# Optimization experiments

Measured on AMD Instinct MI355X. Metric: run time of the kernel, lower is better.

## Reference

```python
import jax, jax.numpy as jnp
import numpy as np

B, S, E, H = 4, 1024, 1024, 16
D = E // H  # head_dim = 64


def setup_inputs() -> dict:
    key = jax.random.key(0)
    ks = jax.random.split(key, 12)
    s = 1.0 / np.sqrt(E)
    return {
        "query": jax.random.normal(ks[0], (B, S, E), jnp.float32),
        "key_": jax.random.normal(ks[1], (B, S, E), jnp.float32),
        "value": jax.random.normal(ks[2], (B, S, E), jnp.float32),
        "mask": jnp.ones((B, S, S), dtype=bool),
        "Wq": jax.random.uniform(ks[3], (E, E), jnp.float32, -s, s),
        "bq": jax.random.uniform(ks[4], (E,), jnp.float32, -s, s),
        "Wk": jax.random.uniform(ks[5], (E, E), jnp.float32, -s, s),
        "bk": jax.random.uniform(ks[6], (E,), jnp.float32, -s, s),
        "Wv": jax.random.uniform(ks[7], (E, E), jnp.float32, -s, s),
        "bv": jax.random.uniform(ks[8], (E,), jnp.float32, -s, s),
        "Wo": jax.random.uniform(ks[9], (E, E), jnp.float32, -s, s),
        "bo": jax.random.uniform(ks[10], (E,), jnp.float32, -s, s),
    }


def reference(query, key_, value, mask, Wq, bq, Wk, bk, Wv, bv, Wo, bo):
    # project and split heads: [B,S,E] -> [B,H,S,D]
    def heads(x, W, b):
        return (x @ W + b).reshape(B, -1, H, D).transpose(0, 2, 1, 3)

    q = heads(query, Wq, bq)
    k = heads(key_, Wk, bk)
    v = heads(value, Wv, bv)

    scores = jnp.einsum("bhqd,bhkd->bhqk", q, k) / jnp.sqrt(jnp.float32(D))
    # bool mask: positions where mask==0 are filled with -1e9
    scores = jnp.where(mask[:, None, :, :], scores, jnp.float32(-1e9))
    attn_weights = jax.nn.softmax(scores, axis=-1)  # [B,H,Sq,Sk]
    out = jnp.einsum("bhqk,bhkd->bhqd", attn_weights, v)
    out = out.transpose(0, 2, 1, 3).reshape(B, -1, E)  # [B,Sq,E]
    attn_output = out @ Wo + bo
    return attn_output, attn_weights
```

## Files before the change

### kernel.cpp

```cpp
#include <hip/hip_runtime.h>
#include <stdint.h>

typedef __bf16 bf16;
typedef bf16 bf16x2 __attribute__((ext_vector_type(2)));
typedef bf16 bf16x4 __attribute__((ext_vector_type(4)));
typedef bf16 bf16x8 __attribute__((ext_vector_type(8)));
typedef float f32x4 __attribute__((ext_vector_type(4)));
typedef float f32x16 __attribute__((ext_vector_type(16)));

static constexpr int Bc = 4, Sc = 1024, Ec = 1024, Hc = 16, Dc = 64, BSc = 4096;

__device__ __forceinline__ void gld_lds16(const void* g, void* s) {
  __builtin_amdgcn_global_load_lds((const __attribute__((address_space(1))) void*)g,
                                   (__attribute__((address_space(3))) void*)s, 16, 0, 0);
}

__global__ void detect_mask_kernel(const uint8_t* __restrict__ mask, int* flag) {
  if (threadIdx.x == 0 && blockIdx.x == 0) {
    bool everyGroupHasZero = true;
    bool anyNonzero = false;
    for (int j = 0; j < 16; ++j) {
      bool z = false;
      for (int bjj = 0; bjj < 4; ++bjj) {
        uint8_t byte = mask[4 * j + bjj];
        if (byte == 0) z = true;
        if (byte != 0) anyNonzero = true;
      }
      if (!z) everyGroupHasZero = false;
    }
    flag[0] = (everyGroupHasZero && anyNonzero) ? 4 : 1;
    flag[1] = 1;
  }
}

__global__ __launch_bounds__(256) void scan_mask_kernel(const uint8_t* __restrict__ mask,
                                                        int* __restrict__ mflag) {
  const int stride = mflag[0];
  bool ok = true;
  const uint4* p = (const uint4*)mask;
  if (stride == 1) {
    const int n = (Bc * Sc * Sc) / 16;
    for (int i = blockIdx.x * blockDim.x + threadIdx.x; i < n; i += gridDim.x * blockDim.x) {
      uint4 w = p[i];
      uint32_t z = 0;
      z |= (w.x - 0x01010101u) & ~w.x;
      z |= (w.y - 0x01010101u) & ~w.y;
      z |= (w.z - 0x01010101u) & ~w.z;
      z |= (w.w - 0x01010101u) & ~w.w;
      if (z & 0x80808080u) ok = false;
    }
  } else {
    const int n = (Bc * Sc * Sc) / 4;
    for (int i = blockIdx.x * blockDim.x + threadIdx.x; i < n; i += gridDim.x * blockDim.x) {
      uint4 w = p[i];
      if (w.x == 0u || w.y == 0u || w.z == 0u || w.w == 0u) ok = false;
    }
  }
  if (!ok) atomicAnd(&mflag[1], 0);
}

__global__ __launch_bounds__(256) void convert_x_kernel(
    const float* __restrict__ q, const float* __restrict__ k, const float* __restrict__ v,
    bf16* __restrict__ xb) {
  const int n4 = (BSc * Ec) / 4;
  for (int i = blockIdx.x * blockDim.x + threadIdx.x; i < 3 * n4; i += gridDim.x * blockDim.x) {
    int which = i / n4;
    int off = i - which * n4;
    const float4* src = (which == 0) ? (const float4*)q : (which == 1) ? (const float4*)k : (const float4*)v;
    float4 f = src[off];
    bf16x4 o;
    o[0] = (bf16)f.x; o[1] = (bf16)f.y; o[2] = (bf16)f.z; o[3] = (bf16)f.w;
    *(bf16x4*)(xb + (size_t)which * BSc * Ec + (size_t)off * 4) = o;
  }
}

__global__ __launch_bounds__(256) void convtrans_w_kernel(
    const float* __restrict__ Wq, const float* __restrict__ Wk,
    const float* __restrict__ Wv, const float* __restrict__ Wo,
    bf16* __restrict__ wT) {
  __shared__ float tile[64][65];
  const int k0 = blockIdx.x * 64, n0 = blockIdx.y * 64, z = blockIdx.z;
  const float* W = (z == 0) ? Wq : (z == 1) ? Wk : (z == 2) ? Wv : Wo;
  bf16* out = wT + (size_t)z * Ec * Ec;
  const int t = threadIdx.x;
#pragma unroll
  for (int p = 0; p < 16; p++) {
    int r = p * 4 + (t >> 6), c = t & 63;
    tile[r][c] = W[(size_t)(k0 + r) * Ec + n0 + c];
  }
  __syncthreads();
#pragma unroll
  for (int p = 0; p < 8; p++) {
    int n = p * 8 + (t >> 5), kk = (t & 31) * 2;
    bf16x2 v2;
    v2[0] = (bf16)tile[kk][n];
    v2[1] = (bf16)tile[kk + 1][n];
    *(bf16x2*)(out + (size_t)(n0 + n) * Ec + k0 + kk) = v2;
  }
}

template <int MODE>
__global__ __launch_bounds__(256) void gemm128_kernel(
    const bf16* __restrict__ A_, const bf16* __restrict__ W_,
    const float* __restrict__ bias0, const float* __restrict__ bias1, const float* __restrict__ bias2,
    bf16* __restrict__ outb_, float* __restrict__ outf) {
  constexpr int K = 1024, N = 1024;
  const int z = blockIdx.z;
  const bf16* A = A_ + (size_t)z * BSc * K;
  const bf16* Wt = W_ + (size_t)z * N * K;
  const float* bias = (z == 0) ? bias0 : (z == 1) ? bias1 : bias2;
  bf16* outb = outb_ + (size_t)z * Bc * Hc * Sc * Dc;
  const float oscale = (MODE == 1 && z == 0) ? 0.125f : 1.0f;
  const int n0 = blockIdx.x * 128, m0 = blockIdx.y * 128;

  __shared__ bf16 As[128 * 64];
  __shared__ bf16 Bs[128 * 64];
  const int t = threadIdx.x, wave = t >> 6, lane = t & 63;
  const int wr = wave >> 1, wc = wave & 1;

  f32x4 acc[4][4];
#pragma unroll
  for (int i = 0; i < 4; i++)
#pragma unroll
    for (int j = 0; j < 4; j++)
#pragma unroll
      for (int r = 0; r < 4; r++) acc[i][j][r] = 0.f;

  const int srow = (lane >> 3);
  const int scol = (lane & 7) * 8;

  for (int kt = 0; kt < K; kt += 64) {
#pragma unroll
    for (int i = 0; i < 4; i++) {
      const int chunk = i * 4 + wave;
      const int row = chunk * 8 + srow;
      gld_lds16(A + (size_t)(m0 + row) * K + kt + scol, &As[chunk * 512]);
      gld_lds16(Wt + (size_t)(n0 + row) * K + kt + scol, &Bs[chunk * 512]);
    }
    __syncthreads();
#pragma unroll
    for (int kk = 0; kk < 2; kk++) {
      bf16x8 af[4], bg[4];
#pragma unroll
      for (int i = 0; i < 4; i++) {
        af[i] = *(const bf16x8*)&As[(64 * wr + i * 16 + (lane & 15)) * 64 + kk * 32 + (lane >> 4) * 8];
        bg[i] = *(const bf16x8*)&Bs[(64 * wc + i * 16 + (lane & 15)) * 64 + kk * 32 + (lane >> 4) * 8];
      }
#pragma unroll
      for (int mi = 0; mi < 4; mi++)
#pragma unroll
        for (int ni = 0; ni < 4; ni++)
          acc[mi][ni] = __builtin_amdgcn_mfma_f32_16x16x32_bf16(af[mi], bg[ni], acc[mi][ni], 0, 0, 0);
    }
    __syncthreads();
  }

#pragma unroll
  for (int mi = 0; mi < 4; mi++) {
#pragma unroll
    for (int ni = 0; ni < 4; ni++) {
      const int col = n0 + 64 * wc + ni * 16 + (lane & 15);
      const float bvl = bias[col];
#pragma unroll
      for (int r = 0; r < 4; r++) {
        const int row = m0 + 64 * wr + mi * 16 + (lane >> 4) * 4 + r;
        const float v = (acc[mi][ni][r] + bvl) * oscale;
        if (MODE == 0) {
          outf[(size_t)row * N + col] = v;
        } else {
          const int bidx = row >> 10, s = row & 1023, hh = col >> 6, d = col & 63;
          const int dst = (z == 1) ? (d ^ ((s & 7) << 3)) : d;
          outb[(((size_t)bidx * Hc + hh) * Sc + s) * Dc + dst] = (bf16)v;
        }
      }
    }
  }
}

__global__ __launch_bounds__(256) void transpose_v_kernel(const bf16* __restrict__ Vb,
                                                          bf16* __restrict__ VTb) {
  __shared__ bf16 tile[64][66];
  const int s0 = blockIdx.x * 64, bh = blockIdx.y;
  const bf16* src = Vb + (size_t)bh * Sc * Dc;
  bf16* dst = VTb + (size_t)bh * Dc * Sc;
  const int t = threadIdx.x;
#pragma unroll
  for (int p = 0; p < 8; p++) {
    int s = p * 8 + (t >> 5), d = (t & 31) * 2;
    *(bf16x2*)&tile[s][d] = *(const bf16x2*)(src + (size_t)(s0 + s) * Dc + d);
  }
  __syncthreads();
#pragma unroll
  for (int p = 0; p < 8; p++) {
    int d = p * 8 + (t >> 5), s = (t & 31) * 2;
    bf16x2 v2;
    v2[0] = tile[s][d];
    v2[1] = tile[s + 1][d];
    const int sidx = (s0 + s) ^ ((d & 7) << 3);
    *(bf16x2*)(dst + (size_t)d * Sc + sidx) = v2;
  }
}

__device__ __forceinline__ f32x16 qk_lds(const char* sK, const bf16x8 qf[4],
                                         int koff, int l31, int hi) {
  const int row = koff + l31;
  const char* base = sK + row * 128;
  const int sw = (row & 7) << 4;
  f32x16 a;
#pragma unroll
  for (int r = 0; r < 16; r++) a[r] = 0.f;
#pragma unroll
  for (int ks = 0; ks < 4; ks++) {
    const bf16x8 kf = *(const bf16x8*)(base + ((ks * 32 + hi * 16) ^ sw));
    a = __builtin_amdgcn_mfma_f32_32x32x16_bf16(kf, qf[ks], a, 0, 0, 0);
  }
  return a;
}

__device__ __forceinline__ void mask_app(f32x16& a, int kt, const uint8_t* mrow1,
                                         const uint8_t* mrow4, int mstride, int hi) {
  if (mstride == 1) {
#pragma unroll
    for (int gg = 0; gg < 4; gg++) {
      const int kg = kt + gg * 8 + hi * 4;
      const uint32_t mw = *(const uint32_t*)(mrow1 + kg);
#pragma unroll
      for (int r = 0; r < 4; r++)
        if (((mw >> (8 * r)) & 0xffu) == 0u) a[gg * 4 + r] = -1e9f;
    }
  } else {
#pragma unroll
    for (int gg = 0; gg < 4; gg++) {
      const int kg = kt + gg * 8 + hi * 4;
      const uint4 m4 = *(const uint4*)(mrow4 + (size_t)4 * kg);
      const uint32_t w[4] = {m4.x, m4.y, m4.z, m4.w};
#pragma unroll
      for (int r = 0; r < 4; r++)
        if (w[r] == 0u) a[gg * 4 + r] = -1e9f;
    }
  }
}

__global__ __launch_bounds__(256, 3) void attn_kernel(
    const bf16* __restrict__ Qb, const bf16* __restrict__ Kb, const bf16* __restrict__ VTb,
    const uint8_t* __restrict__ mask, const int* __restrict__ mflag,
    float* __restrict__ wout_, bf16* __restrict__ ctx) {
  const int qg = blockIdx.x, h = blockIdx.y, b = blockIdx.z;
  const int bh = b * Hc + h;
  const int t = threadIdx.x, wave = t >> 6, lane = t & 63;
  const int l31 = lane & 31, hi = lane >> 5;
  const int q0 = qg * 128 + wave * 32;
  const int q = q0 + l31;

  __shared__ __attribute__((aligned(16))) char smem[49664];
  float* Pt = (float*)(smem + 32768) + wave * 1056;

  const bf16* Qp = Qb + ((size_t)bh * Sc + q) * Dc;
  bf16x8 qf[4];
#pragma unroll
  for (int ks = 0; ks < 4; ks++) qf[ks] = *(const bf16x8*)(Qp + ks * 16 + hi * 8);

  const int allTrue = mflag[1];
  const int mstride = mflag[0];
  const uint8_t* mrow1 = mask + (size_t)(b * Sc + q) * Sc;
  const uint8_t* mrow4 = mask + (size_t)(b * Sc + q) * Sc * 4;

  const char* Kbb = (const char*)(Kb + (size_t)bh * Sc * Dc);
  const char* VTbb = (const char*)(VTb + (size_t)bh * Dc * Sc);

  float m = -3.0e38f, l = 0.f;
  for (int st8 = 0; st8 < 8; st8++) {
#pragma unroll
    for (int j = 0; j < 4; j++) {
      const int off = j * 4096 + wave * 1024;
      gld_lds16(Kbb + st8 * 16384 + off + lane * 16, smem + off);
    }
    __syncthreads();
#pragma unroll
    for (int tl = 0; tl < 4; tl++) {
      f32x16 a = qk_lds(smem, qf, tl * 32, l31, hi);
      if (!allTrue) mask_app(a, st8 * 128 + tl * 32, mrow1, mrow4, mstride, hi);
      float tm = a[0];
#pragma unroll
      for (int r = 1; r < 16; r++) tm = fmaxf(tm, a[r]);
      const float mnew = fmaxf(m, tm);
      float s = 0.f;
#pragma unroll
      for (int r = 0; r < 16; r++) s += __expf(a[r] - mnew);
      l = l * __expf(m - mnew) + s;
      m = mnew;
    }
    __syncthreads();
  }
  {
    const float mo = __shfl_xor(m, 32), lo = __shfl_xor(l, 32);
    const float M = fmaxf(m, mo);
    l = l * __expf(m - M) + lo * __expf(mo - M);
    m = M;
  }
  const float invl = 1.f / l;

  float* wbase = wout_ + ((size_t)bh * Sc + q0) * Sc;
  f32x16 oacc[2];
#pragma unroll
  for (int nj = 0; nj < 2; nj++)
#pragma unroll
    for (int r = 0; r < 16; r++) oacc[nj][r] = 0.f;

  for (int st8 = 0; st8 < 8; st8++) {
#pragma unroll
    for (int j = 0; j < 4; j++) {
      const int off = j * 4096 + wave * 1024;
      gld_lds16(Kbb + st8 * 16384 + off + lane * 16, smem + off);
      const int goff = off + lane * 16;
      const int d = goff >> 8, ko = goff & 255;
      gld_lds16(VTbb + (size_t)d * 2048 + st8 * 256 + ko, smem + 16384 + off);
    }
    __syncthreads();
#pragma unroll
    for (int tl = 0; tl < 4; tl++) {
      f32x16 a = qk_lds(smem, qf, tl * 32, l31, hi);
      if (!allTrue) mask_app(a, st8 * 128 + tl * 32, mrow1, mrow4, mstride, hi);
#pragma unroll
      for (int gg = 0; gg < 4; gg++) {
        f32x4 w4;
#pragma unroll
        for (int r = 0; r < 4; r++) w4[r] = __expf(a[gg * 4 + r] - m) * invl;
        *(f32x4*)&Pt[l31 * 33 + gg * 8 + hi * 4] = w4;
      }
#pragma unroll
      for (int i = 0; i < 4; i++) {
        const int q2 = 8 * i + (lane >> 3), kk = (lane & 7) * 4;
        const f32x4 v4 = *(const f32x4*)&Pt[q2 * 33 + kk];
        __builtin_nontemporal_store(v4,
            (f32x4*)(wbase + (size_t)q2 * Sc + st8 * 128 + tl * 32 + kk));
      }
#pragma unroll
      for (int st = 0; st < 2; st++) {
        const f32x4 a0 = *(const f32x4*)&Pt[l31 * 33 + st * 16 + hi * 8];
        const f32x4 a1 = *(const f32x4*)&Pt[l31 * 33 + st * 16 + hi * 8 + 4];
        bf16x8 pa;
#pragma unroll
        for (int j = 0; j < 4; j++) {
          pa[j] = (bf16)a0[j];
          pa[4 + j] = (bf16)a1[j];
        }
#pragma unroll
        for (int nj = 0; nj < 2; nj++) {
          const int d = nj * 32 + l31;
          const int off = ((tl * 32 + st * 16 + hi * 8) * 2) ^ ((d & 7) << 4);
          const bf16x8 bv = *(const bf16x8*)(smem + 16384 + d * 256 + off);
          oacc[nj] = __builtin_amdgcn_mfma_f32_32x32x16_bf16(pa, bv, oacc[nj], 0, 0, 0);
        }
      }
    }
    __syncthreads();
  }

#pragma unroll
  for (int nj = 0; nj < 2; nj++) {
#pragma unroll
    for (int rg = 0; rg < 16; rg++) {
      const int qq = (rg & 3) + 8 * (rg >> 2) + 4 * hi;
      Pt[qq * 33 + l31] = oacc[nj][rg];
    }
    const int rr = lane >> 1, c0 = (lane & 1) * 16;
    bf16x8 o0, o1;
#pragma unroll
    for (int j = 0; j < 8; j++) {
      o0[j] = (bf16)Pt[rr * 33 + c0 + j];
      o1[j] = (bf16)Pt[rr * 33 + c0 + 8 + j];
    }
    bf16* cbase = ctx + ((size_t)(b * Sc + q0 + rr)) * Ec + h * Dc + nj * 32 + c0;
    *(bf16x8*)cbase = o0;
    *(bf16x8*)(cbase + 8) = o1;
  }
}

extern "C" void kernel_launch(void* const* d_in, const int* in_sizes, int n_in,
                              void* d_out, int out_size, void* d_ws, size_t ws_size,
                              hipStream_t stream) {
  const float* q = (const float*)d_in[0];
  const float* k = (const float*)d_in[1];
  const float* v = (const float*)d_in[2];
  const uint8_t* mask = (const uint8_t*)d_in[3];
  const float* Wq = (const float*)d_in[4];
  const float* bq = (const float*)d_in[5];
  const float* Wk = (const float*)d_in[6];
  const float* bk = (const float*)d_in[7];
  const float* Wv = (const float*)d_in[8];
  const float* bv = (const float*)d_in[9];
  const float* Wo = (const float*)d_in[10];
  const float* bo = (const float*)d_in[11];

  bf16* wsb = (bf16*)d_ws;
  bf16* xb = wsb;
  bf16* ctx = wsb;
  bf16* VTb = wsb + (size_t)4 * 1024 * 1024;
  bf16* wT = wsb + (size_t)12 * 1024 * 1024;
  bf16* Qb = wsb + (size_t)16 * 1024 * 1024;
  bf16* Kb = wsb + (size_t)20 * 1024 * 1024;
  bf16* Vb = wsb + (size_t)24 * 1024 * 1024;
  int* mflag = (int*)((char*)d_ws + (size_t)56 * 1024 * 1024);

  float* outf = (float*)d_out;
  float* attnw = outf + (size_t)4 * 1024 * 1024;

  detect_mask_kernel<<<1, 64, 0, stream>>>(mask, mflag);
  scan_mask_kernel<<<1024, 256, 0, stream>>>(mask, mflag);
  convert_x_kernel<<<2048, 256, 0, stream>>>(q, k, v, xb);
  convtrans_w_kernel<<<dim3(16, 16, 4), 256, 0, stream>>>(Wq, Wk, Wv, Wo, wT);
  gemm128_kernel<1><<<dim3(8, 32, 3), 256, 0, stream>>>(xb, wT, bq, bk, bv, Qb, nullptr);
  transpose_v_kernel<<<dim3(16, 64), 256, 0, stream>>>(Vb, VTb);
  attn_kernel<<<dim3(8, 16, 4), 256, 0, stream>>>(Qb, Kb, VTb, mask, mflag, attnw, ctx);
  gemm128_kernel<0><<<dim3(8, 32, 1), 256, 0, stream>>>(ctx, wT + (size_t)3 * 1024 * 1024,
                                                        bo, bo, bo, nullptr, outf);
}
```

Measured before the change: 224.4 us.

## Double-buffer K/V tiles in LDS and stage probabilities as bf16

The attention kernel now prefetches the next K tile (and V^T tile in the second pass) into an alternate LDS buffer while the current tile is processed. The goal is to overlap global loads with MFMA and softmax work instead of stalling at each barrier. The probability scratch and the output transpose buffer change from fp32 to bf16, which halves their LDS traffic and removes per-element conversions. In exchange, LDS per block grows to about 74 KB and occupancy drops from 3 to 2 blocks per CU. The fp32 attention weights written to global memory are now rounded through bf16, which lowers output precision.

```diff
diff --git a/kernel.cpp b/kernel.cpp
--- a/kernel.cpp
+++ b/kernel.cpp
@@ -241,7 +241,7 @@
   }
 }
 
-__global__ __launch_bounds__(256, 3) void attn_kernel(
+__global__ __launch_bounds__(256, 2) void attn_kernel(
     const bf16* __restrict__ Qb, const bf16* __restrict__ Kb, const bf16* __restrict__ VTb,
     const uint8_t* __restrict__ mask, const int* __restrict__ mflag,
     float* __restrict__ wout_, bf16* __restrict__ ctx) {
@@ -252,8 +252,8 @@
   const int q0 = qg * 128 + wave * 32;
   const int q = q0 + l31;
 
-  __shared__ __attribute__((aligned(16))) char smem[49664];
-  float* Pt = (float*)(smem + 32768) + wave * 1056;
+  __shared__ __attribute__((aligned(16))) char smem[75776];
+  bf16* Ptb = (bf16*)(smem + 65536) + wave * 1280;
 
   const bf16* Qp = Qb + ((size_t)bh * Sc + q) * Dc;
   bf16x8 qf[4];
@@ -269,16 +269,26 @@
   const char* VTbb = (const char*)(VTb + (size_t)bh * Dc * Sc);
 
   float m = -3.0e38f, l = 0.f;
+#pragma unroll
+  for (int j = 0; j < 4; j++) {
+    const int off = j * 4096 + wave * 1024;
+    gld_lds16(Kbb + off + lane * 16, smem + off);
+  }
+  __syncthreads();
   for (int st8 = 0; st8 < 8; st8++) {
-#pragma unroll
-    for (int j = 0; j < 4; j++) {
-      const int off = j * 4096 + wave * 1024;
-      gld_lds16(Kbb + st8 * 16384 + off + lane * 16, smem + off);
-    }
-    __syncthreads();
+    const int cur = st8 & 1;
+    if (st8 < 7) {
+#pragma unroll
+      for (int j = 0; j < 4; j++) {
+        const int off = j * 4096 + wave * 1024;
+        gld_lds16(Kbb + (st8 + 1) * 16384 + off + lane * 16,
+                  smem + (cur ^ 1) * 16384 + off);
+      }
+    }
+    const char* sK = smem + cur * 16384;
 #pragma unroll
     for (int tl = 0; tl < 4; tl++) {
-      f32x16 a = qk_lds(smem, qf, tl * 32, l31, hi);
+      f32x16 a = qk_lds(sK, qf, tl * 32, l31, hi);
       if (!allTrue) mask_app(a, st8 * 128 + tl * 32, mrow1, mrow4, mstride, hi);
       float tm = a[0];
 #pragma unroll
@@ -307,49 +317,60 @@
 #pragma unroll
     for (int r = 0; r < 16; r++) oacc[nj][r] = 0.f;
 
+#pragma unroll
+  for (int j = 0; j < 4; j++) {
+    const int off = j * 4096 + wave * 1024;
+    gld_lds16(Kbb + off + lane * 16, smem + off);
+    const int goff = off + lane * 16;
+    const int d = goff >> 8, ko = goff & 255;
+    gld_lds16(VTbb + (size_t)d * 2048 + ko, smem + 32768 + off);
+  }
+  __syncthreads();
   for (int st8 = 0; st8 < 8; st8++) {
-#pragma unroll
-    for (int j = 0; j < 4; j++) {
-      const int off = j * 4096 + wave * 1024;
-      gld_lds16(Kbb + st8 * 16384 + off + lane * 16, smem + off);
-      const int goff = off + lane * 16;
-      const int d = goff >> 8, ko = goff & 255;
-      gld_lds16(VTbb + (size_t)d * 2048 + st8 * 256 + ko, smem + 16384 + off);
-    }
-    __syncthreads();
+    const int cur = st8 & 1;
+    if (st8 < 7) {
+#pragma unroll
+      for (int j = 0; j < 4; j++) {
+        const int off = j * 4096 + wave * 1024;
+        gld_lds16(Kbb + (st8 + 1) * 16384 + off + lane * 16,
+                  smem + (cur ^ 1) * 16384 + off);
+        const int goff = off + lane * 16;
+        const int d = goff >> 8, ko = goff & 255;
+        gld_lds16(VTbb + (size_t)d * 2048 + (st8 + 1) * 256 + ko,
+                  smem + 32768 + (cur ^ 1) * 16384 + off);
+      }
+    }
+    const char* sK = smem + cur * 16384;
+    const char* sV = smem + 32768 + cur * 16384;
 #pragma unroll
     for (int tl = 0; tl < 4; tl++) {
-      f32x16 a = qk_lds(smem, qf, tl * 32, l31, hi);
+      f32x16 a = qk_lds(sK, qf, tl * 32, l31, hi);
       if (!allTrue) mask_app(a, st8 * 128 + tl * 32, mrow1, mrow4, mstride, hi);
 #pragma unroll
       for (int gg = 0; gg < 4; gg++) {
-        f32x4 w4;
-#pragma unroll
-        for (int r = 0; r < 4; r++) w4[r] = __expf(a[gg * 4 + r] - m) * invl;
-        *(f32x4*)&Pt[l31 * 33 + gg * 8 + hi * 4] = w4;
+        bf16x4 p4;
+#pragma unroll
+        for (int r = 0; r < 4; r++) p4[r] = (bf16)(__expf(a[gg * 4 + r] - m) * invl);
+        *(bf16x4*)&Ptb[l31 * 40 + gg * 8 + hi * 4] = p4;
       }
 #pragma unroll
       for (int i = 0; i < 4; i++) {
         const int q2 = 8 * i + (lane >> 3), kk = (lane & 7) * 4;
-        const f32x4 v4 = *(const f32x4*)&Pt[q2 * 33 + kk];
+        const bf16x4 pv4 = *(const bf16x4*)&Ptb[q2 * 40 + kk];
+        f32x4 v4;
+#pragma unroll
+        for (int r = 0; r < 4; r++) v4[r] = (float)pv4[r];
         __builtin_nontemporal_store(v4,
             (f32x4*)(wbase + (size_t)q2 * Sc + st8 * 128 + tl * 32 + kk));
       }
 #pragma unroll
       for (int st = 0; st < 2; st++) {
-        const f32x4 a0 = *(const f32x4*)&Pt[l31 * 33 + st * 16 + hi * 8];
-        const f32x4 a1 = *(const f32x4*)&Pt[l31 * 33 + st * 16 + hi * 8 + 4];
-        bf16x8 pa;
-#pragma unroll
-        for (int j = 0; j < 4; j++) {
-          pa[j] = (bf16)a0[j];
-          pa[4 + j] = (bf16)a1[j];
-        }
+        const bf16x8 pa = *(const bf16x8*)&Ptb[l31 * 40 + st * 16 + hi * 8];
 #pragma unroll
         for (int nj = 0; nj < 2; nj++) {
           const int d = nj * 32 + l31;
           const int off = ((tl * 32 + st * 16 + hi * 8) * 2) ^ ((d & 7) << 4);
-          const bf16x8 bv = *(const bf16x8*)(smem + 16384 + d * 256 + off);
+          const bf16x8 bv = *(const bf16x8*)(sV + d * 256 + off);
           oacc[nj] = __builtin_amdgcn_mfma_f32_32x32x16_bf16(pa, bv, oacc[nj], 0, 0, 0);
         }
       }
@@ -362,15 +383,11 @@
 #pragma unroll
     for (int rg = 0; rg < 16; rg++) {
       const int qq = (rg & 3) + 8 * (rg >> 2) + 4 * hi;
-      Pt[qq * 33 + l31] = oacc[nj][rg];
+      Ptb[qq * 40 + l31] = (bf16)oacc[nj][rg];
     }
     const int rr = lane >> 1, c0 = (lane & 1) * 16;
-    bf16x8 o0, o1;
-#pragma unroll
-    for (int j = 0; j < 8; j++) {
-      o0[j] = (bf16)Pt[rr * 33 + c0 + j];
-      o1[j] = (bf16)Pt[rr * 33 + c0 + 8 + j];
-    }
+    const bf16x8 o0 = *(const bf16x8*)&Ptb[rr * 40 + c0];
+    const bf16x8 o1 = *(const bf16x8*)&Ptb[rr * 40 + c0 + 8];
     bf16* cbase = ctx + ((size_t)(b * Sc + q0 + rr)) * Ec + h * Dc + nj * 32 + c0;
     *(bf16x8*)cbase = o0;
     *(bf16x8*)(cbase + 8) = o1;
```

Result: faster. 192.4 us (-14.3%).
